# Kernel tuning notes

Measured on AMD Instinct MI355X. Metric: run time of the kernel, lower is better.

## Reference

```python
import jax, jax.numpy as jnp
import numpy as np
from jax import lax

# Hardcoded module constants (from source)
T, B = 8, 64
CIN, C, HW, NCLS = 3, 64, 32, 10
V_INIT, V_DECAY, V_THR = 0.0, 0.8, 1.2


def conv_raw(x, w, b):
    # x: [T, B, Cin, H, W] -> conv2d per timestep, stride 1, pad 1
    t, bsz = x.shape[:2]
    xf = x.reshape((t * bsz,) + x.shape[2:])
    y = lax.conv_general_dilated(
        xf, w, window_strides=(1, 1), padding=[(1, 1), (1, 1)],
        dimension_numbers=('NCHW', 'OIHW', 'NCHW'))
    y = y + b[None, :, None, None]
    return y.reshape((t, bsz) + y.shape[1:])


def lif(i_cur):
    # NOTE: original code reads v[t] from the v_init-initialized tensor each
    # step (not v[t-1]), so there is NO temporal recurrence: v = v_init*decay + I[t]
    v = V_INIT * V_DECAY + i_cur
    return (v >= V_THR).astype(i_cur.dtype)


def setup_inputs() -> dict:
    key = jax.random.key(0)
    ks = jax.random.split(key, 7)
    spike_input = jax.random.uniform(ks[0], (T, B, CIN, HW, HW), jnp.float32)
    # original uses plain torch.randn for weights and biases
    w1 = jax.random.normal(ks[1], (C, CIN, 3, 3), jnp.float32)
    b1 = jax.random.normal(ks[2], (C,), jnp.float32)
    w2 = jax.random.normal(ks[3], (C, C, 3, 3), jnp.float32)
    b2 = jax.random.normal(ks[4], (C,), jnp.float32)
    wfc = jax.random.normal(ks[5], (NCLS, C * HW * HW), jnp.float32)
    bfc = jax.random.normal(ks[6], (NCLS,), jnp.float32)
    return {"spike_input": spike_input, "w1": w1, "b1": b1,
            "w2": w2, "b2": b2, "wfc": wfc, "bfc": bfc}


def reference(spike_input, w1, b1, w2, b2, wfc, bfc):
    x = lif(conv_raw(spike_input, w1, b1))      # [T,B,64,32,32] binary spikes
    x = lif(conv_raw(x, w2, b2))                # [T,B,64,32,32]
    x = x.reshape(T, B, -1)                     # [T,B,64*32*32]
    out = jnp.einsum('tbi,oi->tbo', x, wfc) + bfc
    return out.sum(0)                           # [B, 10]
```

## Files before the change

### kernel.cpp

```cpp
#include <hip/hip_runtime.h>
#include <hip/hip_bf16.h>


typedef __attribute__((ext_vector_type(8))) short bf16x8;
typedef __attribute__((ext_vector_type(4))) float f32x4;
typedef __attribute__((ext_vector_type(4))) int   i32x4;

#define S1Q (5.5f/127.0f)
#define S2Q (S1Q/254.0f)

static const size_t SZ_IMG  = 73984;
static const size_t OFF_S8  = 0;
static const size_t OFF_CNT = 512*SZ_IMG;
static const size_t OFF_W1F = OFF_CNT + (4u<<20);
static const size_t OFF_BQ  = OFF_W1F + 8192;

__global__ __launch_bounds__(256) void kprep(
    const float* __restrict__ w1, const float* __restrict__ w2,
    short* __restrict__ W1F, signed char* __restrict__ Bq)
{
  int i = blockIdx.x*256 + threadIdx.x;
  if (i < 4096) {
    int t2 = i >> 11, r = i & 2047, co = r >> 5, k = r & 31;
    short out = 0;
    if (k < 27) {
      int s = k/3, ci = k - s*3;
      float w = w1[co*27 + ci*9 + s];
      __hip_bfloat16 h = __float2bfloat16(w);
      if (t2 == 0) out = *(short*)&h;
      else { __hip_bfloat16 lo = __float2bfloat16(w - (float)h); out = *(short*)&lo; }
    }
    W1F[i] = out;
  }
  if (i < 36864) {
    int co = i/576, rem = i - co*576, ci = rem/9, s = rem - ci*9;
    float w = w2[i];
    int q1 = (int)roundf(w * (1.0f/S1Q)); q1 = q1 > 127 ? 127 : (q1 < -127 ? -127 : q1);
    float r1 = w - S1Q*(float)q1;
    int q2 = (int)roundf(r1 * (1.0f/S2Q)); q2 = q2 > 127 ? 127 : (q2 < -127 ? -127 : q2);
    int off = s*4096 + co*64 + ci;
    Bq[off] = (signed char)q1; Bq[36864 + off] = (signed char)q2;
  }
}

__global__ __launch_bounds__(256) void rz(unsigned char* __restrict__ S8)
{
  unsigned char* base = S8 + (size_t)blockIdx.x * SZ_IMG;
  for (int i = threadIdx.x; i < 2112; i += 256) {
    int off;
    if (i < 544)       off = i*4;
    else if (i < 1088) off = 33*2176 + (i-544)*4;
    else { int k = i - 1088; int r = 1 + (k>>5); int j = k & 31;
           off = r*2176 + ((j < 16) ? j*4 : 33*64 + (j-16)*4); }
    *(unsigned int*)(base + off) = 0u;
  }
}

__global__ __launch_bounds__(256, 2) void conv1_k(
    const float* __restrict__ x, const short* __restrict__ W1F,
    const float* __restrict__ b1, unsigned char* __restrict__ S8)
{
  const int img = blockIdx.x;
  const int tid = threadIdx.x;
  const int w   = tid >> 6;
  const int l   = tid & 63;
  const int lm  = l & 15, lk = l >> 4;

  __shared__ int xt4[7344];
  __shared__ i32x4 bnc4[4][16][4];
  unsigned short* xs = (unsigned short*)xt4;
  unsigned char*  bnc = (unsigned char*)bnc4;

  for (int i = tid; i < 7344; i += 256) xt4[i] = 0;
  __syncthreads();
  const float* xin = x + (size_t)img * 3072;
  for (int j = tid; j < 3072; j += 256) {
    int ci = j >> 10, r = (j >> 5) & 31, c = j & 31;
    float f = xin[j];
    __hip_bfloat16 h = __float2bfloat16(f);
    __hip_bfloat16 lo = __float2bfloat16(f - (float)h);
    int idx = ci*1224 + (r+1)*36 + (c+1);
    xs[idx] = *(unsigned short*)&h;
    xs[idx + 7344] = *(unsigned short*)&lo;
  }
  __syncthreads();

  bf16x8 Wf[2][4];
  float  b1v[4];
  #pragma unroll
  for (int t2 = 0; t2 < 2; t2++)
    #pragma unroll
    for (int nf = 0; nf < 4; nf++)
      Wf[t2][nf] = *(const bf16x8*)(W1F + t2*2048 + (nf*16+lm)*32 + lk*8);
  #pragma unroll
  for (int nf = 0; nf < 4; nf++) b1v[nf] = b1[nf*16 + lm];

  int off16[8];
  #pragma unroll
  for (int e = 0; e < 8; e++) {
    int k = lk*8 + e;
    if (k < 27) { int s = k/3, ci = k - s*3, dr = s/3, dc = s - dr*3;
                  off16[e] = ci*1224 + dr*36 + dc; }
    else off16[e] = 0;
  }

  unsigned char* S8b = S8 + (size_t)img * SZ_IMG;
  for (int fi = 0; fi < 16; fi++) {
    const int pxF = w*16 + fi;
    const int row = pxF >> 1, colh = pxF & 1;
    const int base16 = row*36 + colh*16 + lm;
    bf16x8 ah, al;
    #pragma unroll
    for (int e = 0; e < 8; e++) {
      int idx = base16 + off16[e];
      ah[e] = (short)xs[idx];
      al[e] = (short)xs[idx + 7344];
    }
    f32x4 acc[4] = {};
    #pragma unroll
    for (int nf = 0; nf < 4; nf++) {
      acc[nf] = __builtin_amdgcn_mfma_f32_16x16x32_bf16(ah, Wf[0][nf], acc[nf], 0,0,0);
      acc[nf] = __builtin_amdgcn_mfma_f32_16x16x32_bf16(al, Wf[0][nf], acc[nf], 0,0,0);
      acc[nf] = __builtin_amdgcn_mfma_f32_16x16x32_bf16(ah, Wf[1][nf], acc[nf], 0,0,0);
      acc[nf] = __builtin_amdgcn_mfma_f32_16x16x32_bf16(al, Wf[1][nf], acc[nf], 0,0,0);
    }
    #pragma unroll
    for (int nf = 0; nf < 4; nf++)
      #pragma unroll
      for (int e4 = 0; e4 < 4; e4++) {
        float v = acc[nf][e4] + b1v[nf];
        bnc[w*1024 + (lk*4+e4)*64 + nf*16 + lm] = (v >= 1.2f) ? 1 : 0;
      }
    const int pxl = l >> 2, coq = l & 3;
    i32x4 sp = *(const i32x4*)(bnc + w*1024 + pxl*64 + coq*16);
    const int colp = colh*16 + pxl + 1;
    const int cq = coq ^ ((colp >> 1) & 3);
    *(i32x4*)(S8b + ((row+1)*34 + colp)*64 + cq*16) = sp;
  }
}

__global__ __launch_bounds__(512, 2) void conv2_k(
    const unsigned char* __restrict__ S8, const signed char* __restrict__ Bq,
    const float* __restrict__ b2, unsigned char* __restrict__ cnt)
{
  __shared__ __align__(16) unsigned char Abuf[40960];
  const int j = blockIdx.x;
  const int xcd = j & 7, g = j >> 3;
  const int b   = ((g & 7) << 3) | xcd;
  const int sub = g >> 3;
  const int rh  = sub >> 1, ch = sub & 1;

  const int tid = threadIdx.x;
  const int w = tid >> 6, l = tid & 63;
  const int lm = l & 15, lk = l >> 4;

  i32x4 Bf[2][9][2];
  #pragma unroll
  for (int q = 0; q < 2; q++)
    #pragma unroll
    for (int s = 0; s < 9; s++)
      #pragma unroll
      for (int nf = 0; nf < 2; nf++)
        Bf[q][s][nf] = *(const i32x4*)(Bq + q*36864 + s*4096 + (ch*32+nf*16+lm)*64 + lk*16);

  const float b2v[2] = { b2[ch*32 + lm], b2[ch*32 + 16 + lm] };

  unsigned int cntp[4][2] = {};

  for (int t = 0; t < 8; t++) {
    const unsigned char* As = S8 + (size_t)(t*64 + b)*SZ_IMG + (size_t)rh*34816;
    #pragma unroll
    for (int it = 0; it < 5; it++) {
      const int idx = it*512 + tid;
      *(i32x4*)(Abuf + idx*16) = *(const i32x4*)(As + (size_t)idx*16);
    }
    __syncthreads();

    i32x4 acc1[4][2] = {}, acc2[4][2] = {};
    #pragma unroll
    for (int s = 0; s < 9; s++) {
      const int dr = s/3, dc = s - dr*3;
      #pragma unroll
      for (int a = 0; a < 4; a++) {
        const int tr = w*2 + (a>>1) + dr;
        const int cp = ((a&1)<<4) + lm + dc;
        i32x4 Af = *(const i32x4*)(Abuf + tr*2176 + cp*64 + ((lk ^ ((cp>>1)&3))<<4));
        #pragma unroll
        for (int nf = 0; nf < 2; nf++) {
          acc1[a][nf] = __builtin_amdgcn_mfma_i32_16x16x64_i8(Af, Bf[0][s][nf], acc1[a][nf],0,0,0);
          acc2[a][nf] = __builtin_amdgcn_mfma_i32_16x16x64_i8(Af, Bf[1][s][nf], acc2[a][nf],0,0,0);
        }
      }
    }

    #pragma unroll
    for (int a = 0; a < 4; a++)
      #pragma unroll
      for (int nf = 0; nf < 2; nf++) {
        unsigned int p = 0;
        #pragma unroll
        for (int e = 0; e < 4; e++) {
          float v = S1Q*(float)acc1[a][nf][e] + S2Q*(float)acc2[a][nf][e] + b2v[nf];
          p |= (v >= 1.2f ? 1u : 0u) << (8*e);
        }
        cntp[a][nf] += p;
      }
    __syncthreads();
  }

  #pragma unroll
  for (int a = 0; a < 4; a++) {
    const int row  = rh*16 + w*2 + (a>>1);
    const int colb = ((a&1)<<4) + lk*4;
    #pragma unroll
    for (int nf = 0; nf < 2; nf++) {
      const int co = ch*32 + nf*16 + lm;
      *(unsigned int*)(cnt + ((size_t)(b*64 + co))*1024 + row*32 + colb) = cntp[a][nf];
    }
  }
}

__global__ __launch_bounds__(256) void fc_k(
    const unsigned char* __restrict__ cnt, const float* __restrict__ wfc,
    const float* __restrict__ bfc, float* __restrict__ out)
{
  const int b = blockIdx.x & 63;
  const int chunk = blockIdx.x >> 6;
  const int tid = threadIdx.x;
  float acc[10];
  #pragma unroll
  for (int o = 0; o < 10; o++) acc[o] = 0.f;
  const int i4base = chunk*4096 + tid;
  for (int w = 0; w < 16; w++) {
    int i4 = i4base + w*256;
    uchar4 cv = *(const uchar4*)(cnt + (size_t)b*65536 + i4*4);
    float c0 = cv.x, c1 = cv.y, c2 = cv.z, c3 = cv.w;
    #pragma unroll
    for (int o = 0; o < 10; o++) {
      float4 wv = *(const float4*)(wfc + (size_t)o*65536 + i4*4);
      acc[o] += wv.x*c0 + wv.y*c1 + wv.z*c2 + wv.w*c3;
    }
  }
  __shared__ float red[10][256];
  #pragma unroll
  for (int o = 0; o < 10; o++) red[o][tid] = acc[o];
  __syncthreads();
  for (int off = 128; off > 0; off >>= 1) {
    if (tid < off) {
      #pragma unroll
      for (int o = 0; o < 10; o++) red[o][tid] += red[o][tid + off];
    }
    __syncthreads();
  }
  if (tid < 10) {
    float v = red[tid][0];
    if (chunk == 0) v += 8.0f * bfc[tid];
    atomicAdd(out + b*10 + tid, v);
  }
}

extern "C" void kernel_launch(void* const* d_in, const int* in_sizes, int n_in,
                              void* d_out, int out_size, void* d_ws, size_t ws_size,
                              hipStream_t stream)
{
  const float* x   = (const float*)d_in[0];
  const float* w1  = (const float*)d_in[1];
  const float* b1  = (const float*)d_in[2];
  const float* w2  = (const float*)d_in[3];
  const float* b2  = (const float*)d_in[4];
  const float* wfc = (const float*)d_in[5];
  const float* bfc = (const float*)d_in[6];
  float* out = (float*)d_out;

  unsigned char* ws  = (unsigned char*)d_ws;
  unsigned char* S8  = ws + OFF_S8;
  unsigned char* cnt = ws + OFF_CNT;
  short*         W1F = (short*)(ws + OFF_W1F);
  signed char*   Bq  = (signed char*)(ws + OFF_BQ);

  rz<<<512, 256, 0, stream>>>(S8);
  hipMemsetAsync(out, 0, 64*10*sizeof(float), stream);
  kprep<<<144, 256, 0, stream>>>(w1, w2, W1F, Bq);
  conv1_k<<<512, 256, 0, stream>>>(x, W1F, b1, S8);
  conv2_k<<<256, 512, 0, stream>>>(S8, Bq, b2, cnt);
  fc_k<<<256, 256, 0, stream>>>(cnt, wfc, bfc, out);
}
```

Before: 154.3 us.

## Double-buffer conv2 LDS tiles via direct global-to-LDS loads, drop halo padding kernel

conv1 now writes unpadded 32x32 spike images, and the separate zeroing kernel for the padding border is removed. conv2 re-tiles work so each block handles 8 output rows and all 64 channels, split across wave groups. It zeroes an LDS halo once, then prefetches the next timestep's rows into a second LDS buffer with global_load_lds while the current timestep's MFMAs run. Output counts are staged through LDS so global stores are coalesced 16-byte writes. The double buffer adds LDS pressure and depends on the halo zeros never being overwritten.

```diff
diff --git a/kernel.cpp b/kernel.cpp
--- a/kernel.cpp
+++ b/kernel.cpp
@@ -9,11 +9,19 @@
 #define S1Q (5.5f/127.0f)
 #define S2Q (S1Q/254.0f)
 
-static const size_t SZ_IMG  = 73984;
+static const size_t SZ_IMG  = 65536;
 static const size_t OFF_S8  = 0;
 static const size_t OFF_CNT = 512*SZ_IMG;
 static const size_t OFF_W1F = OFF_CNT + (4u<<20);
 static const size_t OFF_BQ  = OFF_W1F + 8192;
+
+#define SWZ(cp) (((cp) >> 1) & 3)
+
+__device__ __forceinline__ void gl_lds16(const void* g, void* l) {
+  __builtin_amdgcn_global_load_lds(
+      (const __attribute__((address_space(1))) unsigned int*)g,
+      (__attribute__((address_space(3))) unsigned int*)l, 16, 0, 0);
+}
 
 __global__ __launch_bounds__(256) void kprep(
     const float* __restrict__ w1, const float* __restrict__ w2,
@@ -43,19 +51,6 @@
   }
 }
 
-__global__ __launch_bounds__(256) void rz(unsigned char* __restrict__ S8)
-{
-  unsigned char* base = S8 + (size_t)blockIdx.x * SZ_IMG;
-  for (int i = threadIdx.x; i < 2112; i += 256) {
-    int off;
-    if (i < 544)       off = i*4;
-    else if (i < 1088) off = 33*2176 + (i-544)*4;
-    else { int k = i - 1088; int r = 1 + (k>>5); int j = k & 31;
-           off = r*2176 + ((j < 16) ? j*4 : 33*64 + (j-16)*4); }
-    *(unsigned int*)(base + off) = 0u;
-  }
-}
-
 __global__ __launch_bounds__(256, 2) void conv1_k(
     const float* __restrict__ x, const short* __restrict__ W1F,
     const float* __restrict__ b1, unsigned char* __restrict__ S8)
@@ -133,9 +128,9 @@
       }
     const int pxl = l >> 2, coq = l & 3;
     i32x4 sp = *(const i32x4*)(bnc + w*1024 + pxl*64 + coq*16);
-    const int colp = colh*16 + pxl + 1;
-    const int cq = coq ^ ((colp >> 1) & 3);
-    *(i32x4*)(S8b + ((row+1)*34 + colp)*64 + cq*16) = sp;
+    const int gcol = colh*16 + pxl;
+    const int cq = coq ^ SWZ(gcol + 1);
+    *(i32x4*)(S8b + (size_t)(row*32 + gcol)*64 + cq*16) = sp;
   }
 }
 
@@ -143,16 +138,15 @@
     const unsigned char* __restrict__ S8, const signed char* __restrict__ Bq,
     const float* __restrict__ b2, unsigned char* __restrict__ cnt)
 {
-  __shared__ __align__(16) unsigned char Abuf[40960];
-  const int j = blockIdx.x;
-  const int xcd = j & 7, g = j >> 3;
-  const int b   = ((g & 7) << 3) | xcd;
-  const int sub = g >> 3;
-  const int rh  = sub >> 1, ch = sub & 1;
-
+  __shared__ __align__(16) unsigned char Abuf[2][21760];
+  const int j  = blockIdx.x;
+  const int b  = ((j >> 3) & 7) * 8 + (j & 7);
+  const int rq = j >> 6;
   const int tid = threadIdx.x;
-  const int w = tid >> 6, l = tid & 63;
+  const int wv = tid >> 6, l = tid & 63;
   const int lm = l & 15, lk = l >> 4;
+  const int ch = wv >> 2;
+  const int wr = wv & 3;
 
   i32x4 Bf[2][9][2];
   #pragma unroll
@@ -162,29 +156,63 @@
       #pragma unroll
       for (int nf = 0; nf < 2; nf++)
         Bf[q][s][nf] = *(const i32x4*)(Bq + q*36864 + s*4096 + (ch*32+nf*16+lm)*64 + lk*16);
-
   const float b2v[2] = { b2[ch*32 + lm], b2[ch*32 + 16 + lm] };
 
+  {
+    i32x4 z = {0,0,0,0};
+    i32x4* ap = (i32x4*)Abuf;
+    #pragma unroll
+    for (int it = 0; it < 6; it++) { int c = it*512 + tid; if (c < 2720) ap[c] = z; }
+  }
+  __syncthreads();
+
+  {
+    const unsigned char* Simg = S8 + (size_t)(0*64 + b)*SZ_IMG;
+    if (wv < 5) {
+      #pragma unroll
+      for (int rr = 0; rr < 2; rr++) {
+        const int lr = wv*2 + rr;
+        const int grow = rq*8 - 1 + lr;
+        if (grow >= 0 && grow < 32) {
+          const unsigned char* src = Simg + grow*2048 + l*16;
+          unsigned char* dst = &Abuf[0][lr*2176 + 64];
+          gl_lds16(src, dst);
+          gl_lds16(src + 1024, dst + 1024);
+        }
+      }
+    }
+  }
+  __syncthreads();
+
   unsigned int cntp[4][2] = {};
 
   for (int t = 0; t < 8; t++) {
-    const unsigned char* As = S8 + (size_t)(t*64 + b)*SZ_IMG + (size_t)rh*34816;
-    #pragma unroll
-    for (int it = 0; it < 5; it++) {
-      const int idx = it*512 + tid;
-      *(i32x4*)(Abuf + idx*16) = *(const i32x4*)(As + (size_t)idx*16);
-    }
-    __syncthreads();
-
+    if (t < 7 && wv < 5) {
+      const unsigned char* Simg = S8 + (size_t)((t+1)*64 + b)*SZ_IMG;
+      unsigned char* bufn = Abuf[(t+1) & 1];
+      #pragma unroll
+      for (int rr = 0; rr < 2; rr++) {
+        const int lr = wv*2 + rr;
+        const int grow = rq*8 - 1 + lr;
+        if (grow >= 0 && grow < 32) {
+          const unsigned char* src = Simg + grow*2048 + l*16;
+          unsigned char* dst = bufn + lr*2176 + 64;
+          gl_lds16(src, dst);
+          gl_lds16(src + 1024, dst + 1024);
+        }
+      }
+    }
+
+    const unsigned char* ab = Abuf[t & 1];
     i32x4 acc1[4][2] = {}, acc2[4][2] = {};
     #pragma unroll
     for (int s = 0; s < 9; s++) {
       const int dr = s/3, dc = s - dr*3;
       #pragma unroll
       for (int a = 0; a < 4; a++) {
-        const int tr = w*2 + (a>>1) + dr;
+        const int lr = 2*wr + (a>>1) + dr;
         const int cp = ((a&1)<<4) + lm + dc;
-        i32x4 Af = *(const i32x4*)(Abuf + tr*2176 + cp*64 + ((lk ^ ((cp>>1)&3))<<4));
+        i32x4 Af = *(const i32x4*)(ab + lr*2176 + cp*64 + ((lk ^ SWZ(cp)) << 4));
         #pragma unroll
         for (int nf = 0; nf < 2; nf++) {
           acc1[a][nf] = __builtin_amdgcn_mfma_i32_16x16x64_i8(Af, Bf[0][s][nf], acc1[a][nf],0,0,0);
@@ -208,15 +236,24 @@
     __syncthreads();
   }
 
+  unsigned char* bb = (unsigned char*)Abuf;
   #pragma unroll
   for (int a = 0; a < 4; a++) {
-    const int row  = rh*16 + w*2 + (a>>1);
+    const int orow = 2*wr + (a>>1);
     const int colb = ((a&1)<<4) + lk*4;
     #pragma unroll
     for (int nf = 0; nf < 2; nf++) {
       const int co = ch*32 + nf*16 + lm;
-      *(unsigned int*)(cnt + ((size_t)(b*64 + co))*1024 + row*32 + colb) = cntp[a][nf];
-    }
+      *(unsigned int*)(bb + co*256 + orow*32 + colb) = cntp[a][nf];
+    }
+  }
+  __syncthreads();
+  #pragma unroll
+  for (int it = 0; it < 2; it++) {
+    const int c = it*512 + tid;
+    const int co = c >> 4, inner = (c & 15) << 4;
+    *(i32x4*)(cnt + (size_t)(b*64 + co)*1024 + rq*256 + inner) =
+        *(const i32x4*)(bb + co*256 + inner);
   }
 }
 
@@ -278,7 +315,6 @@
   short*         W1F = (short*)(ws + OFF_W1F);
   signed char*   Bq  = (signed char*)(ws + OFF_BQ);
 
-  rz<<<512, 256, 0, stream>>>(S8);
   hipMemsetAsync(out, 0, 64*10*sizeof(float), stream);
   kprep<<<144, 256, 0, stream>>>(w1, w2, W1F, Bq);
   conv1_k<<<512, 256, 0, stream>>>(x, W1F, b1, S8);
```

After: 143.7 us. 1.07x faster.
